# Kernel optimization log

Hardware: AMD Instinct MI355X
Metric: run time of the kernel (lower is better)

Reference implementation:

```python
import jax, jax.numpy as jnp
import numpy as np

N_NODES = 51200      # 128 graphs * 400 ROIs
N_ROI = 400
HID = 64             # 'batch_size' arg of the torch module = hidden channels = n_timepoints
N_EDGES = 1638400    # avg degree 32
N_CLASSES = 2
NEG_SLOPE = 0.01


def setup_inputs():
    key = jax.random.key(0)
    ks = jax.random.split(key, 20)
    s = 0.05
    inp = {
        'x': jax.random.normal(ks[0], (N_NODES, HID), dtype=jnp.float32),
        'edge_index': jax.random.randint(ks[1], (2, N_EDGES), 0, N_NODES, dtype=jnp.int64),
        'edge_weight': jax.random.uniform(ks[2], (N_EDGES,), dtype=jnp.float32),
        # GCNConv weights stored [in, out]; biases [out]
        'W1': jax.random.normal(ks[3], (HID, HID), dtype=jnp.float32) * s,
        'b1': jnp.zeros((HID,), jnp.float32),
        'W2': jax.random.normal(ks[4], (HID, HID), dtype=jnp.float32) * s,
        'b2': jnp.zeros((HID,), jnp.float32),
        'W3': jax.random.normal(ks[5], (HID, HID), dtype=jnp.float32) * s,
        'b3': jnp.zeros((HID,), jnp.float32),
        'W4': jax.random.normal(ks[6], (HID, HID), dtype=jnp.float32) * s,
        'b4': jnp.zeros((HID,), jnp.float32),
        'fc1_w': jax.random.normal(ks[7], (N_ROI * HID, 256), dtype=jnp.float32) * 0.01,
        'fc1_b': jnp.zeros((256,), jnp.float32),
        'fc2_w': jax.random.normal(ks[8], (256, 128), dtype=jnp.float32) * s,
        'fc2_b': jnp.zeros((128,), jnp.float32),
        'fc3_w': jax.random.normal(ks[9], (128, N_CLASSES), dtype=jnp.float32) * s,
        'fc3_b': jnp.zeros((N_CLASSES,), jnp.float32),
    }
    return inp


def _gcn_norm(edge_index, edge_weight, n):
    # PyG GCNConv: add self-loops (weight 1), symmetric D^-1/2 A D^-1/2 normalization
    loop = jnp.arange(n, dtype=edge_index.dtype)
    src = jnp.concatenate([edge_index[0], loop])
    dst = jnp.concatenate([edge_index[1], loop])
    w = jnp.concatenate([edge_weight, jnp.ones((n,), edge_weight.dtype)])
    deg = jax.ops.segment_sum(w, dst, num_segments=n)
    dis = jnp.where(deg > 0, jax.lax.rsqrt(jnp.maximum(deg, 1e-30)), 0.0)
    norm = dis[src] * w * dis[dst]
    return src, dst, norm


def _conv(h, W, b, src, dst, norm, n):
    h = h @ W                                   # [N, out]
    msg = h[src] * norm[:, None]                # gather + scale
    out = jax.ops.segment_sum(msg, dst, num_segments=n) + b
    return out


def _leaky(v):
    return jnp.where(v >= 0, v, NEG_SLOPE * v)


def _head(h, fc1_w, fc1_b, fc2_w, fc2_b, fc3_w, fc3_b):
    # global_mean_pool with batch = arange(N) is identity; pool == reshape to graphs
    g = h.reshape(-1, N_ROI * HID)              # [G, n_roi*hid]
    g = g @ fc1_w + fc1_b                       # dropout is eval-mode identity
    g = g @ fc2_w + fc2_b
    g = g @ fc3_w + fc3_b
    return g


def reference(x, edge_index, edge_weight, W1, b1, W2, b2, W3, b3, W4, b4,
              fc1_w, fc1_b, fc2_w, fc2_b, fc3_w, fc3_b):
    n = x.shape[0]
    src, dst, norm = _gcn_norm(edge_index, edge_weight, n)
    h = _leaky(_conv(x, W1, b1, src, dst, norm, n))
    h = _leaky(_conv(h, W2, b2, src, dst, norm, n))
    h = _leaky(_conv(h, W3, b3, src, dst, norm, n))
    h = _leaky(_conv(h, W4, b4, src, dst, norm, n))
    logits = _head(h, fc1_w, fc1_b, fc2_w, fc2_b, fc3_w, fc3_b)
    logits0 = _head(x, fc1_w, fc1_b, fc2_w, fc2_b, fc3_w, fc3_b)
    penal = 0.09 * logits.shape[0] / jnp.linalg.norm(logits - logits0)
    return logits, penal
```

## Files before the change

kernel.cpp:

```cpp
#include <hip/hip_runtime.h>
#include <cstddef>

#define N_NODES 51200
#define N_EDGES 1638400
#define HID 64
#define N_ROI 400
#define N_GRAPHS 128
#define KHEAD 25600
#define NEG_SLOPE 0.01f
#define CAP 80
#define NCHUNK 200
#define CHUNK 8192
#define NBIN 1024
#define BINSZ 50
#define LSTRIDE 81
#define NWC 400

typedef unsigned short u16;
typedef unsigned int u32;
typedef unsigned char u8;
typedef float f32x2 __attribute__((ext_vector_type(2)));

__device__ inline u16 f2bf(float f) {
    u32 u = __float_as_uint(f);
    u32 r = u + 0x7FFFu + ((u >> 16) & 1u);
    return (u16)(r >> 16);
}
__device__ inline float bf2f(u16 h) { return __uint_as_float(((u32)h) << 16); }

__device__ inline f32x2 dec8lo(u32 v) { return __builtin_amdgcn_cvt_pk_f32_fp8((int)v, false); }
__device__ inline f32x2 dec8hi(u32 v) { return __builtin_amdgcn_cvt_pk_f32_fp8((int)v, true); }
template <bool HI>
__device__ inline u32 enc8(float a, float b, u32 old) {
    return (u32)__builtin_amdgcn_cvt_pk_fp8_f32(a, b, (int)old, HI);
}
__device__ inline u32 pack4_fp8(float a, float b, float c, float d) {
    u32 w = enc8<false>(a, b, 0u);
    return enc8<true>(c, d, w);
}


__global__ __launch_bounds__(1024) void k1(const int* __restrict__ ei,
                                           const float* __restrict__ ew,
                                           uint2* __restrict__ chunkData,
                                           u32* __restrict__ offcnt,
                                           const float* __restrict__ x,
                                           u8* __restrict__ x8,
                                           const float* __restrict__ fc2w,
                                           const float* __restrict__ fc3w,
                                           const float* __restrict__ fc1b,
                                           const float* __restrict__ fc2b,
                                           const float* __restrict__ fc3b,
                                           float* __restrict__ fc23,
                                           float* __restrict__ bc,
                                           float* __restrict__ sq,
                                           int* __restrict__ done) {
    int bid = blockIdx.x, t = threadIdx.x;
    __shared__ u32 cnt[NBIN];
    __shared__ u32 cur[NBIN];
    __shared__ u32 wsum[16];
    __shared__ uint2 stag[CHUNK];
    __shared__ float t1[128];

    if (bid < NCHUNK) {
        cnt[t] = 0;
        __syncthreads();
        int base = bid * CHUNK;
        const int4* sp = reinterpret_cast<const int4*>(ei + base);
        const int4* dp = reinterpret_cast<const int4*>(ei + N_EDGES + base);
        const float4* wp = reinterpret_cast<const float4*>(ew + base);
        int4 sa = sp[2 * t], sb = sp[2 * t + 1];
        int4 da = dp[2 * t], db = dp[2 * t + 1];
        float4 wa = wp[2 * t], wb = wp[2 * t + 1];
        int ss[8] = {sa.x, sa.y, sa.z, sa.w, sb.x, sb.y, sb.z, sb.w};
        int dd[8] = {da.x, da.y, da.z, da.w, db.x, db.y, db.z, db.w};
        float wv[8] = {wa.x, wa.y, wa.z, wa.w, wb.x, wb.y, wb.z, wb.w};
        u32 lo[8]; int bin[8];
        #pragma unroll
        for (int i = 0; i < 8; i++) {
            int b = (int)((u32)dd[i] / BINSZ);
            bin[i] = b;
            lo[i] = (u32)ss[i] | ((u32)(dd[i] - b * BINSZ) << 16);
            atomicAdd(&cnt[b], 1u);
        }
        __syncthreads();
        int wave = t >> 6, lane = t & 63;
        u32 v = cnt[t], inc = v;
        #pragma unroll
        for (int d = 1; d < 64; d <<= 1) {
            u32 o = __shfl_up(inc, d, 64);
            if (lane >= d) inc += o;
        }
        if (lane == 63) wsum[wave] = inc;
        __syncthreads();
        if (t == 0) {
            u32 r = 0;
            #pragma unroll
            for (int i = 0; i < 16; i++) { u32 c = wsum[i]; wsum[i] = r; r += c; }
        }
        __syncthreads();
        u32 excl = inc - v + wsum[wave];
        cur[t] = excl;
        offcnt[(size_t)bid * NBIN + t] = excl | (v << 16);
        __syncthreads();
        #pragma unroll
        for (int i = 0; i < 8; i++) {
            u32 pos = atomicAdd(&cur[bin[i]], 1u);
            stag[pos] = make_uint2(lo[i], __float_as_uint(wv[i]));
        }
        __syncthreads();
        const uint4* sg4 = reinterpret_cast<const uint4*>(stag);
        uint4* out4 = reinterpret_cast<uint4*>(chunkData + (size_t)base);
        #pragma unroll
        for (int i = 0; i < 4; i++) out4[i * 1024 + t] = sg4[i * 1024 + t];
    } else if (bid < 400) {
        int idx = (bid - NCHUNK) * 1024 + t;
        const float4* xp = reinterpret_cast<const float4*>(x) + (size_t)idx * 4;
        float4 a = xp[0], b = xp[1], c = xp[2], d = xp[3];
        reinterpret_cast<uint4*>(x8)[idx] =
            make_uint4(pack4_fp8(a.x, a.y, a.z, a.w), pack4_fp8(b.x, b.y, b.z, b.w),
                       pack4_fp8(c.x, c.y, c.z, c.w), pack4_fp8(d.x, d.y, d.z, d.w));
    } else {
        if (t == 256) *sq = 0.f;
        if (t == 257) *done = 0;
        if (t < 256) {
            float s0 = 0.f, s1 = 0.f;
            const float* row = fc2w + t * 128;
            for (int j = 0; j < 128; j++) {
                float a = row[j];
                s0 += a * fc3w[2 * j];
                s1 += a * fc3w[2 * j + 1];
            }
            fc23[2 * t] = s0;
            fc23[2 * t + 1] = s1;
        }
        if (t < 128) {
            float s = fc2b[t];
            for (int k = 0; k < 256; k++) s += fc1b[k] * fc2w[k * 128 + t];
            t1[t] = s;
        }
        __syncthreads();
        if (t < 2) {
            float s = fc3b[t];
            for (int j = 0; j < 128; j++) s += t1[j] * fc3w[2 * j + t];
            bc[t] = s;
        }
    }
}


__global__ __launch_bounds__(256) void k1t(const u32* __restrict__ in,
                                           u32* __restrict__ outT) {
    __shared__ u32 tile[32][33];
    int bx = blockIdx.x & 31, cy = blockIdx.x >> 5;
    int b0 = bx * 32, c0 = cy * 32;
    int tx = threadIdx.x & 31, ty = threadIdx.x >> 5;
    for (int i = ty; i < 32; i += 8) {
        int c = c0 + i;
        if (c < NCHUNK) tile[i][tx] = in[(size_t)c * NBIN + b0 + tx];
    }
    __syncthreads();
    for (int i = ty; i < 32; i += 8) {
        int b = b0 + i;
        int c = c0 + tx;
        if (c < NCHUNK) outT[(size_t)b * NCHUNK + c] = tile[tx][i];
    }
}


__global__ __launch_bounds__(512) void k2(const uint2* __restrict__ chunkData,
                                          const u32* __restrict__ offcntT,
                                          u32* __restrict__ buck,
                                          int* __restrict__ cnts,
                                          float* __restrict__ dis,
                                          const float* __restrict__ fc1w,
                                          const float* __restrict__ fc23,
                                          float* __restrict__ Wc) {
    int bid = blockIdx.x, t = threadIdx.x;
    __shared__ u32 lbuck[BINSZ * LSTRIDE];
    __shared__ u32 lcnt[BINSZ];
    __shared__ float ldeg[BINSZ];
    __shared__ u32 oc[NCHUNK];

    if (bid < NBIN) {
        if (t < BINSZ) { lcnt[t] = 0; ldeg[t] = 0.f; }
        if (t < NCHUNK) oc[t] = offcntT[(size_t)bid * NCHUNK + t];
        __syncthreads();
        int w = t >> 6, lane = t & 63;
        int sBase = w * 25;
        for (int j = 0; j < 32; j += 8) {
            int so = j + (lane >> 3);
            int s = sBase + so;
            int i0 = lane & 7;
            int k = 0, off = 0;
            if (so < 25) {
                u32 o = oc[s];
                off = (int)(o & 0xffffu);
                k = (int)(o >> 16);
            }
            const uint2* cd = chunkData + (size_t)s * CHUNK + off;
            for (int i = i0; i < k; i += 8) {
                uint2 e = cd[i];
                u32 node = e.x >> 16;
                u32 src = e.x & 0xffffu;
                float ww = __uint_as_float(e.y);
                u32 pos = atomicAdd(&lcnt[node], 1u);
                if (pos < CAP - 1) lbuck[node * LSTRIDE + pos] = ((u32)f2bf(ww) << 16) | src;
                atomicAdd(&ldeg[node], ww);
            }
        }
        __syncthreads();
        int sg = t >> 5, ln = t & 31;
        for (int n = sg; n < BINSZ; n += 16) {
            int node = bid * BINSZ + n;
            int k = min((int)lcnt[n], CAP - 1);
            u32* dst = buck + (size_t)node * CAP;
            for (int i = ln; i < k; i += 32) dst[i] = lbuck[n * LSTRIDE + i];
            if (ln == 0) {
                cnts[node] = k;
                dis[node] = rsqrtf(1.f + ldeg[n]);
            }
        }
    } else {
        float* f23 = (float*)lbuck;
        f23[t] = fc23[t];
        __syncthreads();
        const float2* f2p = reinterpret_cast<const float2*>(f23);
        int row = (bid - NBIN) * 64 + (t >> 3);
        int p = t & 7;
        const float4* rp = reinterpret_cast<const float4*>(fc1w + (size_t)row * 256 + p * 32);
        float s0 = 0.f, s1 = 0.f;
        #pragma unroll
        for (int i = 0; i < 8; i++) {
            float4 a = rp[i];
            int kb = p * 32 + i * 4;
            float2 w0 = f2p[kb], w1 = f2p[kb + 1], w2 = f2p[kb + 2], w3 = f2p[kb + 3];
            s0 += a.x * w0.x + a.y * w1.x + a.z * w2.x + a.w * w3.x;
            s1 += a.x * w0.y + a.y * w1.y + a.z * w2.y + a.w * w3.y;
        }
        #pragma unroll
        for (int off = 4; off; off >>= 1) {
            s0 += __shfl_down(s0, off, 8);
            s1 += __shfl_down(s1, off, 8);
        }
        if (p == 0) reinterpret_cast<float2*>(Wc)[row] = make_float2(s0, s1);
    }
}


__global__ __launch_bounds__(1024) void k3(u32* __restrict__ buck,
                                           int* __restrict__ cnts,
                                           const float* __restrict__ dis) {
    int gt = blockIdx.x * 1024 + threadIdx.x;
    int node = gt >> 5, sub = gt & 31;
    float d = dis[node];
    int k = cnts[node];
    u32* bk = buck + (size_t)node * CAP;
    for (int j = sub; j < k; j += 32) {
        u32 e = bk[j];
        float val = bf2f((u16)(e >> 16)) * d * dis[e & 0xffffu];
        bk[j] = ((u32)f2bf(val) << 16) | (e & 0xffffu);
    }
    if (sub == 0) {
        bk[k] = ((u32)f2bf(d * d) << 16) | (u32)node;
        cnts[node] = k + 1;
    }
}


__global__ __launch_bounds__(512) void k_layer(const u8* __restrict__ H8,
                                               const u32* __restrict__ buck,
                                               const int* __restrict__ cnts,
                                               const float* __restrict__ W,
                                               const float* __restrict__ bias,
                                               u8* __restrict__ Hout) {
    __shared__ float Ws[64][64];
    __shared__ float ZsT[64][65];
    int t = threadIdx.x;
    int base = blockIdx.x * 64;

    #pragma unroll
    for (int i = 0; i < 2; i++) {
        int f = t + i * 512;
        int kk = f >> 4, c4 = f & 15;
        float4 wv = reinterpret_cast<const float4*>(W)[f];
        *reinterpret_cast<float4*>(&Ws[kk][c4 * 4]) = wv;
    }

    int grp = t >> 3, sub = t & 7;
    int node = base + grp;
    int k = cnts[node];
    const u32* bk = buck + (size_t)node * CAP;
    const uint2* H64 = reinterpret_cast<const uint2*>(H8);
    float a0 = 0.f, a1 = 0.f, a2 = 0.f, a3 = 0.f;
    float a4 = 0.f, a5 = 0.f, a6 = 0.f, a7 = 0.f;
    for (int j0 = 0; j0 < k; j0 += 8) {
        int idx = j0 + sub;
        u32 pre = (idx < k) ? bk[idx] : 0u;
        #pragma unroll
        for (int i = 0; i < 8; i++) {
            u32 e = (u32)__shfl((int)pre, i, 8);
            float val = __uint_as_float(e & 0xffff0000u);
            u32 src = e & 0xffffu;
            uint2 r = H64[(size_t)src * 8 + sub];
            f32x2 l0 = dec8lo(r.x), h0 = dec8hi(r.x);
            f32x2 l1 = dec8lo(r.y), h1 = dec8hi(r.y);
            a0 += val * l0.x; a1 += val * l0.y; a2 += val * h0.x; a3 += val * h0.y;
            a4 += val * l1.x; a5 += val * l1.y; a6 += val * h1.x; a7 += val * h1.y;
        }
    }
    ZsT[8 * sub + 0][grp] = a0; ZsT[8 * sub + 1][grp] = a1;
    ZsT[8 * sub + 2][grp] = a2; ZsT[8 * sub + 3][grp] = a3;
    ZsT[8 * sub + 4][grp] = a4; ZsT[8 * sub + 5][grp] = a5;
    ZsT[8 * sub + 6][grp] = a6; ZsT[8 * sub + 7][grp] = a7;
    __syncthreads();

    int rp2 = t >> 4, c4i = t & 15;
    int r0 = rp2 * 2, c0 = c4i * 4;
    float4 acc0 = {0,0,0,0}, acc1 = {0,0,0,0};
    #pragma unroll 8
    for (int kk = 0; kk < 64; kk++) {
        float z0 = ZsT[kk][r0];
        float z1 = ZsT[kk][r0 + 1];
        float4 w = *reinterpret_cast<const float4*>(&Ws[kk][c0]);
        acc0.x += z0 * w.x; acc0.y += z0 * w.y; acc0.z += z0 * w.z; acc0.w += z0 * w.w;
        acc1.x += z1 * w.x; acc1.y += z1 * w.y; acc1.z += z1 * w.z; acc1.w += z1 * w.w;
    }
    float4 bb = *reinterpret_cast<const float4*>(bias + c0);
    float v0 = acc0.x + bb.x, v1 = acc0.y + bb.y, v2 = acc0.z + bb.z, v3 = acc0.w + bb.w;
    float v4 = acc1.x + bb.x, v5 = acc1.y + bb.y, v6 = acc1.z + bb.z, v7 = acc1.w + bb.w;
    v0 = v0 >= 0.f ? v0 : NEG_SLOPE * v0;
    v1 = v1 >= 0.f ? v1 : NEG_SLOPE * v1;
    v2 = v2 >= 0.f ? v2 : NEG_SLOPE * v2;
    v3 = v3 >= 0.f ? v3 : NEG_SLOPE * v3;
    v4 = v4 >= 0.f ? v4 : NEG_SLOPE * v4;
    v5 = v5 >= 0.f ? v5 : NEG_SLOPE * v5;
    v6 = v6 >= 0.f ? v6 : NEG_SLOPE * v6;
    v7 = v7 >= 0.f ? v7 : NEG_SLOPE * v7;
    u32* outp = reinterpret_cast<u32*>(Hout);
    outp[(size_t)(base + r0) * 16 + c4i]     = pack4_fp8(v0, v1, v2, v3);
    outp[(size_t)(base + r0 + 1) * 16 + c4i] = pack4_fp8(v4, v5, v6, v7);
}


__global__ __launch_bounds__(256) void k_logits(const u8* __restrict__ h4,
                                                const float* __restrict__ x,
                                                const float* __restrict__ Wc,
                                                const float* __restrict__ bc,
                                                float* __restrict__ out,
                                                float* __restrict__ sq,
                                                int* __restrict__ done) {
    int g = blockIdx.x, t = threadIdx.x;
    const u8* bh = h4 + (size_t)g * KHEAD;
    const float* bx = x + (size_t)g * KHEAD;
    float aH0 = 0.f, aH1 = 0.f, aX0 = 0.f, aX1 = 0.f;
    for (int k2 = t; k2 < KHEAD / 2; k2 += 256) {
        u32 hv = reinterpret_cast<const u16*>(bh)[k2];
        f32x2 h = dec8lo(hv);
        float2 xv = reinterpret_cast<const float2*>(bx)[k2];
        float4 wc = reinterpret_cast<const float4*>(Wc)[k2];
        aH0 += h.x * wc.x + h.y * wc.z;
        aH1 += h.x * wc.y + h.y * wc.w;
        aX0 += xv.x * wc.x + xv.y * wc.z;
        aX1 += xv.x * wc.y + xv.y * wc.w;
    }
    for (int off = 32; off > 0; off >>= 1) {
        aH0 += __shfl_down(aH0, off);
        aH1 += __shfl_down(aH1, off);
        aX0 += __shfl_down(aX0, off);
        aX1 += __shfl_down(aX1, off);
    }
    __shared__ float red[4][4];
    int wave = t >> 6, lane = t & 63;
    if (lane == 0) {
        red[wave][0] = aH0; red[wave][1] = aH1;
        red[wave][2] = aX0; red[wave][3] = aX1;
    }
    __syncthreads();
    if (t == 0) {
        float h0 = red[0][0] + red[1][0] + red[2][0] + red[3][0];
        float h1 = red[0][1] + red[1][1] + red[2][1] + red[3][1];
        float x0 = red[0][2] + red[1][2] + red[2][2] + red[3][2];
        float x1 = red[0][3] + red[1][3] + red[2][3] + red[3][3];
        out[2 * g]     = h0 + bc[0];
        out[2 * g + 1] = h1 + bc[1];
        float d0 = h0 - x0, d1 = h1 - x1;
        atomicAdd(sq, d0 * d0 + d1 * d1);
        __threadfence();
        int c = atomicAdd(done, 1);
        if (c == N_GRAPHS - 1) {
            __threadfence();
            float s = atomicAdd(sq, 0.f);
            out[2 * N_GRAPHS] = 0.09f * (float)N_GRAPHS / sqrtf(s);
        }
    }
}


extern "C" void kernel_launch(void* const* d_in, const int* in_sizes, int n_in,
                              void* d_out, int out_size, void* d_ws, size_t ws_size,
                              hipStream_t stream) {
    const float* x    = (const float*)d_in[0];
    const int*   ei   = (const int*)d_in[1];
    const float* ew   = (const float*)d_in[2];
    const float* W1   = (const float*)d_in[3];
    const float* b1   = (const float*)d_in[4];
    const float* W2   = (const float*)d_in[5];
    const float* b2   = (const float*)d_in[6];
    const float* W3   = (const float*)d_in[7];
    const float* b3   = (const float*)d_in[8];
    const float* W4   = (const float*)d_in[9];
    const float* b4   = (const float*)d_in[10];
    const float* fc1w = (const float*)d_in[11];
    const float* fc1b = (const float*)d_in[12];
    const float* fc2w = (const float*)d_in[13];
    const float* fc2b = (const float*)d_in[14];
    const float* fc3w = (const float*)d_in[15];
    const float* fc3b = (const float*)d_in[16];
    float* out = (float*)d_out;

    char* base = (char*)d_ws;
    size_t off = 0;
    auto alloc = [&](size_t bytes) -> void* {
        void* p = base + off;
        off += (bytes + 255) & ~(size_t)255;
        return p;
    };
    uint2* chunkData = (uint2*)alloc((size_t)N_EDGES * 8);
    u32*   offcnt    = (u32*)alloc((size_t)NCHUNK * NBIN * 4);
    u32*   offcntT   = (u32*)alloc((size_t)NCHUNK * NBIN * 4);
    u32*   buck      = (u32*)alloc((size_t)N_NODES * CAP * 4);
    int*   cnts      = (int*)alloc((size_t)N_NODES * 4);
    float* dis       = (float*)alloc((size_t)N_NODES * 4);
    u8*    x8        = (u8*)alloc((size_t)N_NODES * HID);
    u8*    ha        = (u8*)alloc((size_t)N_NODES * HID);
    u8*    hb        = (u8*)alloc((size_t)N_NODES * HID);
    float* fc23      = (float*)alloc(512 * 4);
    float* bc        = (float*)alloc(2 * 4);
    float* Wc        = (float*)alloc((size_t)KHEAD * 2 * 4);
    char*  ctrl      = (char*)alloc(256);
    float* sq        = (float*)ctrl;
    int*   done      = (int*)(ctrl + 4);

    k1<<<401, 1024, 0, stream>>>(ei, ew, chunkData, offcnt, x, x8,
                                 fc2w, fc3w, fc1b, fc2b, fc3b, fc23, bc, sq, done);
    k1t<<<224, 256, 0, stream>>>(offcnt, offcntT);
    k2<<<NBIN + NWC, 512, 0, stream>>>(chunkData, offcntT, buck, cnts, dis,
                                       fc1w, fc23, Wc);
    k3<<<1600, 1024, 0, stream>>>(buck, cnts, dis);

    const float* Wl[4] = {W1, W2, W3, W4};
    const float* bl[4] = {b1, b2, b3, b4};
    u8* hbufs[2] = {ha, hb};
    const u8* hin = x8;
    for (int l = 0; l < 4; l++) {
        u8* hout = hbufs[l & 1];
        k_layer<<<N_NODES / 64, 512, 0, stream>>>(hin, buck, cnts,
                                                  Wl[l], bl[l], hout);
        hin = hout;
    }

    k_logits<<<N_GRAPHS, 256, 0, stream>>>(hin, x, Wc, bc, out, sq, done);
}
```

Baseline: 175.0 us.

## Widen layer gathers to 16-byte loads with two edges per lane group

The per-node aggregation in k_layer now splits the 8 lanes of each node into two halves of 4. Each lane loads 16 bytes (a uint4) of the FP8 feature row, so each half covers a full 64-wide row and the two halves process alternate edges. Partial sums are combined with a shuffle-xor before writing to shared memory. This halves the number of gather iterations per edge batch and uses wider loads, at the cost of 16 accumulators per lane and an extra reduction. Separately, the self-loop entry and incremented count are now written in the bucketing kernel instead of in k3, removing a dependent write step from k3.

```diff
diff --git a/kernel.cpp b/kernel.cpp
--- a/kernel.cpp
+++ b/kernel.cpp
@@ -217,8 +217,10 @@
             u32* dst = buck + (size_t)node * CAP;
             for (int i = ln; i < k; i += 32) dst[i] = lbuck[n * LSTRIDE + i];
             if (ln == 0) {
-                cnts[node] = k;
-                dis[node] = rsqrtf(1.f + ldeg[n]);
+                float d = rsqrtf(1.f + ldeg[n]);
+                dis[node] = d;
+                cnts[node] = k + 1;
+                dst[k] = ((u32)f2bf(d * d) << 16) | (u32)node;
             }
         }
     } else {
@@ -249,21 +251,17 @@
 
 
 __global__ __launch_bounds__(1024) void k3(u32* __restrict__ buck,
-                                           int* __restrict__ cnts,
+                                           const int* __restrict__ cnts,
                                            const float* __restrict__ dis) {
     int gt = blockIdx.x * 1024 + threadIdx.x;
     int node = gt >> 5, sub = gt & 31;
     float d = dis[node];
-    int k = cnts[node];
+    int kk = cnts[node];
     u32* bk = buck + (size_t)node * CAP;
-    for (int j = sub; j < k; j += 32) {
+    for (int j = sub; j < kk - 1; j += 32) {
         u32 e = bk[j];
         float val = bf2f((u16)(e >> 16)) * d * dis[e & 0xffffu];
         bk[j] = ((u32)f2bf(val) << 16) | (e & 0xffffu);
-    }
-    if (sub == 0) {
-        bk[k] = ((u32)f2bf(d * d) << 16) | (u32)node;
-        cnts[node] = k + 1;
     }
 }
 
@@ -288,31 +286,45 @@
     }
 
     int grp = t >> 3, sub = t & 7;
+    int q = sub & 3, hi = sub >> 2;
     int node = base + grp;
     int k = cnts[node];
     const u32* bk = buck + (size_t)node * CAP;
-    const uint2* H64 = reinterpret_cast<const uint2*>(H8);
-    float a0 = 0.f, a1 = 0.f, a2 = 0.f, a3 = 0.f;
-    float a4 = 0.f, a5 = 0.f, a6 = 0.f, a7 = 0.f;
+    const uint4* H128 = reinterpret_cast<const uint4*>(H8);
+    float a[16];
+    #pragma unroll
+    for (int c = 0; c < 16; c++) a[c] = 0.f;
     for (int j0 = 0; j0 < k; j0 += 8) {
         int idx = j0 + sub;
         u32 pre = (idx < k) ? bk[idx] : 0u;
         #pragma unroll
-        for (int i = 0; i < 8; i++) {
-            u32 e = (u32)__shfl((int)pre, i, 8);
+        for (int i = 0; i < 4; i++) {
+            u32 e0 = (u32)__shfl((int)pre, 2 * i, 8);
+            u32 e1 = (u32)__shfl((int)pre, 2 * i + 1, 8);
+            u32 e = hi ? e1 : e0;
             float val = __uint_as_float(e & 0xffff0000u);
             u32 src = e & 0xffffu;
-            uint2 r = H64[(size_t)src * 8 + sub];
-            f32x2 l0 = dec8lo(r.x), h0 = dec8hi(r.x);
-            f32x2 l1 = dec8lo(r.y), h1 = dec8hi(r.y);
-            a0 += val * l0.x; a1 += val * l0.y; a2 += val * h0.x; a3 += val * h0.y;
-            a4 += val * l1.x; a5 += val * l1.y; a6 += val * h1.x; a7 += val * h1.y;
-        }
-    }
-    ZsT[8 * sub + 0][grp] = a0; ZsT[8 * sub + 1][grp] = a1;
-    ZsT[8 * sub + 2][grp] = a2; ZsT[8 * sub + 3][grp] = a3;
-    ZsT[8 * sub + 4][grp] = a4; ZsT[8 * sub + 5][grp] = a5;
-    ZsT[8 * sub + 6][grp] = a6; ZsT[8 * sub + 7][grp] = a7;
+            uint4 r = H128[(size_t)src * 4 + q];
+            f32x2 p0 = dec8lo(r.x), p1 = dec8hi(r.x);
+            f32x2 p2 = dec8lo(r.y), p3 = dec8hi(r.y);
+            f32x2 p4 = dec8lo(r.z), p5 = dec8hi(r.z);
+            f32x2 p6 = dec8lo(r.w), p7 = dec8hi(r.w);
+            a[0]  += val * p0.x; a[1]  += val * p0.y;
+            a[2]  += val * p1.x; a[3]  += val * p1.y;
+            a[4]  += val * p2.x; a[5]  += val * p2.y;
+            a[6]  += val * p3.x; a[7]  += val * p3.y;
+            a[8]  += val * p4.x; a[9]  += val * p4.y;
+            a[10] += val * p5.x; a[11] += val * p5.y;
+            a[12] += val * p6.x; a[13] += val * p6.y;
+            a[14] += val * p7.x; a[15] += val * p7.y;
+        }
+    }
+    #pragma unroll
+    for (int c = 0; c < 16; c++) a[c] += __shfl_xor(a[c], 4, 8);
+    if (hi == 0) {
+        #pragma unroll
+        for (int c = 0; c < 16; c++) ZsT[16 * q + c][grp] = a[c];
+    }
     __syncthreads();
 
     int rp2 = t >> 4, c4i = t & 15;
```

New measurement: 185.2 us. 1.06x slower.
